# Performance work log

Measured on AMD Instinct MI355X. Metric: run time of the kernel, lower is better.

## Reference

```python
import jax, jax.numpy as jnp
import numpy as np

NOPE = 128          # qk_nope_head_dim
ROPE = 64           # qk_rope_head_dim
KV_LORA = 512       # kv_lora_rank
SCALE = (KV_LORA + ROPE) ** (-0.5)


def setup_inputs() -> dict:
    key = jax.random.key(0)
    k1, k2, k3, k4, k5 = jax.random.split(key, 5)
    T, H, K, S = 512, 128, 512, 8192
    q = jax.random.normal(k1, (T, H, NOPE + ROPE), dtype=jnp.float32)
    kv_cache = jax.random.normal(k2, (S, KV_LORA + ROPE), dtype=jnp.float32)
    topk_indices = jax.random.randint(k3, (T, K), 0, S, dtype=jnp.int32)
    k_b_proj_trans = jax.random.normal(k4, (H, KV_LORA, NOPE), dtype=jnp.float32) * 0.02
    v_b_proj = jax.random.normal(k5, (H, 128, KV_LORA), dtype=jnp.float32) * 0.02
    return {"q": q, "kv_cache": kv_cache, "topk_indices": topk_indices,
            "k_b_proj_trans": k_b_proj_trans, "v_b_proj": v_b_proj}


def reference(q, kv_cache, topk_indices, k_b_proj_trans, v_b_proj):
    # q: [T, H, 192]; kv_cache: [S, 576]; topk_indices: [T, K]
    q_nope, q_rope = q[..., :NOPE], q[..., NOPE:]
    # bmm_out(q_nope_t, k_b_proj_trans.transpose(1,2)): [T,H,128] x [H,512,128] -> [T,H,512]
    q_lat = jnp.einsum('thd,hkd->thk', q_nope, k_b_proj_trans)
    q_concat = jnp.concatenate([q_lat, q_rope], axis=-1)        # [T, H, 576]
    # sparse MLA: gather selected latent KV per token
    kv_sel = kv_cache[topk_indices]                              # [T, K, 576]
    scores = jnp.einsum('thc,tkc->thk', q_concat, kv_sel) * SCALE
    p = jax.nn.softmax(scores, axis=-1)                          # [T, H, K]
    attn_lat = jnp.einsum('thk,tkc->thc', p, kv_sel[..., :KV_LORA])  # [T, H, 512]
    # bmm_out(attn_lat_t, v_b_proj.transpose(1,2)): [T,H,512] x [H,512,128] -> [T,H,128]
    out = jnp.einsum('thc,hvc->thv', attn_lat, v_b_proj)
    return out
```

## Files before the change

kernel.cpp:

```cpp
#include <hip/hip_runtime.h>
#include <stdint.h>


#define SCALE 0.041666666666666664f

typedef __bf16 bf16x8 __attribute__((ext_vector_type(8)));
typedef float floatx4 __attribute__((ext_vector_type(4)));
typedef unsigned int uint32x2 __attribute__((ext_vector_type(2)));
typedef unsigned int uint32x4 __attribute__((ext_vector_type(4)));

static __device__ __forceinline__ unsigned short f2bf(float f) {
  unsigned int u = __builtin_bit_cast(unsigned int, f);
  u += 0x7FFF + ((u >> 16) & 1);
  return (unsigned short)(u >> 16);
}
static __device__ __forceinline__ float bf2f(unsigned short h) {
  unsigned int u = ((unsigned int)h) << 16;
  return __builtin_bit_cast(float, u);
}
static __device__ __forceinline__ unsigned int pack2(float lo, float hi) {
  return (unsigned int)f2bf(lo) | ((unsigned int)f2bf(hi) << 16);
}
static __device__ __forceinline__ void ldsdma16(const void* g, void* l) {
  __builtin_amdgcn_global_load_lds(
      (const __attribute__((address_space(1))) void*)g,
      (__attribute__((address_space(3))) void*)l, 16, 0, 0);
}
static __device__ __forceinline__ void issue_fence() {
  asm volatile("" ::: "memory");
  __builtin_amdgcn_sched_barrier(0);
}
static __device__ __forceinline__ unsigned int lds_addr(const void* p) {
  return (unsigned int)(unsigned long long)(
      (__attribute__((address_space(3))) const void*)p);
}
#define TR64(dst, addr, OFF) \
  asm volatile("ds_read_b64_tr_b16 %0, %1 offset:" OFF : "=v"(dst) : "v"(addr))

static __device__ __forceinline__ void stage8_f32(const float* __restrict__ src,
                                                  unsigned short* dst) {
  const float4* s4 = reinterpret_cast<const float4*>(src);
  float4 v0 = s4[0], v1 = s4[1];
  uint4 o;
  o.x = pack2(v0.x, v0.y); o.y = pack2(v0.z, v0.w);
  o.z = pack2(v1.x, v1.y); o.w = pack2(v1.z, v1.w);
  *reinterpret_cast<uint4*>(dst) = o;
}

static __device__ __forceinline__ void mfma_4x4(const unsigned short* As,
                                                const unsigned short* Bs,
                                                int wm, int wn, int l15, int quad,
                                                floatx4 acc[4][4]) {
  bf16x8 af[4], bfr[4];
#pragma unroll
  for (int i = 0; i < 4; ++i)
    af[i] = *reinterpret_cast<const bf16x8*>(&As[(wm + i * 16 + l15) * 32 + quad * 8]);
#pragma unroll
  for (int j = 0; j < 4; ++j)
    bfr[j] = *reinterpret_cast<const bf16x8*>(&Bs[(wn + j * 16 + l15) * 32 + quad * 8]);
#pragma unroll
  for (int i = 0; i < 4; ++i)
#pragma unroll
    for (int j = 0; j < 4; ++j)
      acc[i][j] = __builtin_amdgcn_mfma_f32_16x16x32_bf16(af[i], bfr[j], acc[i][j], 0, 0, 0);
}

__global__ void prep(const float* __restrict__ kv, unsigned short* __restrict__ kvb,
                     const float* __restrict__ q, unsigned short* __restrict__ qc2) {
  int b = blockIdx.x;
  if (b < 4608) {
    int i = b * 256 + threadIdx.x;
    float4 v = reinterpret_cast<const float4*>(kv)[i];
    ushort4 o;
    o.x = f2bf(v.x); o.y = f2bf(v.y); o.z = f2bf(v.z); o.w = f2bf(v.w);
    reinterpret_cast<ushort4*>(kvb)[i] = o;
  } else {
    int i = (b - 4608) * 256 + threadIdx.x;
    int r = i & 63;
    int th = i >> 6;
    int t = th >> 7, h = th & 127;
    qc2[(((size_t)t * 18 + 16 + (r >> 5)) * 128 + h) * 32 + (r & 31)] =
        f2bf(q[(size_t)th * 192 + 128 + r] * SCALE);
  }
}

__global__ __launch_bounds__(256) void qlat_gemm(const float* __restrict__ q,
                                                 const float* __restrict__ kb,
                                                 unsigned short* __restrict__ qc2) {
  const int h = blockIdx.x;
  const int tm = (blockIdx.y & 3) * 128;
  const int tn = (blockIdx.y >> 2) * 128;
  __shared__ __align__(16) unsigned short As[128 * 32];
  __shared__ __align__(16) unsigned short Bs[128 * 32];
  const int tid = threadIdx.x;
  const int lane = tid & 63, wave = tid >> 6;
  const int wm = (wave & 1) * 64, wn = (wave >> 1) * 64;
  const int l15 = lane & 15, quad = lane >> 4;
  const int r0 = tid >> 2, cg = tid & 3;
  const float* a0 = q + ((size_t)(tm + r0) * 128 + h) * 192 + cg * 8;
  const float* a1 = q + ((size_t)(tm + r0 + 64) * 128 + h) * 192 + cg * 8;
  const float* b0 = kb + ((size_t)h * 512 + tn + r0) * 128 + cg * 8;
  const float* b1 = b0 + (size_t)64 * 128;
  floatx4 acc[4][4] = {};
  for (int ks = 0; ks < 4; ++ks) {
    stage8_f32(a0 + ks * 32, &As[tid * 8]);
    stage8_f32(a1 + ks * 32, &As[2048 + tid * 8]);
    stage8_f32(b0 + ks * 32, &Bs[tid * 8]);
    stage8_f32(b1 + ks * 32, &Bs[2048 + tid * 8]);
    __syncthreads();
    mfma_4x4(As, Bs, wm, wn, l15, quad, acc);
    __syncthreads();
  }
#pragma unroll
  for (int i = 0; i < 4; ++i) {
    const int row = wm + i * 16 + quad * 4;
#pragma unroll
    for (int j = 0; j < 4; ++j) {
      const int c = tn + wn + j * 16 + l15;
      const int ks2 = c >> 5, kk = c & 31;
#pragma unroll
      for (int r = 0; r < 4; ++r) {
        const int t = tm + row + r;
        qc2[(((size_t)t * 18 + ks2) * 128 + h) * 32 + kk] = f2bf(acc[i][j][r] * SCALE);
      }
    }
  }
}

__global__ __launch_bounds__(512) void scores_fused(const unsigned short* __restrict__ qc2,
                                                    const unsigned short* __restrict__ kvb,
                                                    const int* __restrict__ topk,
                                                    unsigned short* __restrict__ P2) {
  const int t = blockIdx.x;
  __shared__ __align__(16) unsigned short Bs[3][512 * 32];
  __shared__ __align__(16) float redmx[128][4];
  __shared__ __align__(16) float redsm[128][4];
  const int tid = threadIdx.x;
  const int lane = tid & 63, wave = tid >> 6;
  const int wm2 = (wave >> 2) * 64;
  const int wkn = (wave & 3) * 128;
  const int l15 = lane & 15, quad = lane >> 4;
  const int keyD = tid >> 2;
  const int cD = (tid & 3) * 8;
  const int* tkrow = topk + t * 512;
  const int gi0 = tkrow[0 * 128 + keyD];
  const int gi1 = tkrow[1 * 128 + keyD];
  const int gi2 = tkrow[2 * 128 + keyD];
  const int gi3 = tkrow[3 * 128 + keyD];
  const unsigned short* g0 = kvb + (size_t)gi0 * 576 + cD;
  const unsigned short* g1 = kvb + (size_t)gi1 * 576 + cD;
  const unsigned short* g2 = kvb + (size_t)gi2 * 576 + cD;
  const unsigned short* g3 = kvb + (size_t)gi3 * 576 + cD;
  const unsigned short* aab =
      qc2 + ((size_t)t * 2304 + wm2 + l15) * 32 + quad * 8;
  floatx4 acc[4][8] = {};
  ldsdma16(g0, &Bs[0][0 * 4096 + tid * 8]);
  ldsdma16(g1, &Bs[0][1 * 4096 + tid * 8]);
  ldsdma16(g2, &Bs[0][2 * 4096 + tid * 8]);
  ldsdma16(g3, &Bs[0][3 * 4096 + tid * 8]);
  issue_fence();
  ldsdma16(g0 + 32, &Bs[1][0 * 4096 + tid * 8]);
  ldsdma16(g1 + 32, &Bs[1][1 * 4096 + tid * 8]);
  ldsdma16(g2 + 32, &Bs[1][2 * 4096 + tid * 8]);
  ldsdma16(g3 + 32, &Bs[1][3 * 4096 + tid * 8]);
  issue_fence();
  bf16x8 af[4], an[4];
#pragma unroll
  for (int i = 0; i < 4; ++i)
    af[i] = *reinterpret_cast<const bf16x8*>(aab + i * 512);
  int bi = 0, bn = 2;
  for (int ks = 0; ks < 18; ++ks) {
    asm volatile("s_waitcnt vmcnt(8)" ::: "memory");
    __builtin_amdgcn_s_barrier();
    if (ks < 16) {
      ldsdma16(g0 + (ks + 2) * 32, &Bs[bn][0 * 4096 + tid * 8]);
      ldsdma16(g1 + (ks + 2) * 32, &Bs[bn][1 * 4096 + tid * 8]);
      ldsdma16(g2 + (ks + 2) * 32, &Bs[bn][2 * 4096 + tid * 8]);
      ldsdma16(g3 + (ks + 2) * 32, &Bs[bn][3 * 4096 + tid * 8]);
      issue_fence();
    }
    if (ks < 17) {
#pragma unroll
      for (int i = 0; i < 4; ++i)
        an[i] = *reinterpret_cast<const bf16x8*>(
            aab + (size_t)(ks + 1) * 4096 + i * 512);
    }
    bf16x8 bfr[8];
#pragma unroll
    for (int j = 0; j < 8; ++j)
      bfr[j] = *reinterpret_cast<const bf16x8*>(
          &Bs[bi][(wkn + j * 16 + l15) * 32 + quad * 8]);
#pragma unroll
    for (int i = 0; i < 4; ++i)
#pragma unroll
      for (int j = 0; j < 8; ++j)
        acc[i][j] =
            __builtin_amdgcn_mfma_f32_16x16x32_bf16(af[i], bfr[j], acc[i][j], 0, 0, 0);
#pragma unroll
    for (int i = 0; i < 4; ++i) af[i] = an[i];
    bi = bi == 2 ? 0 : bi + 1;
    bn = bn == 2 ? 0 : bn + 1;
  }
  float fm[4][4], inv[4][4];
#pragma unroll
  for (int i = 0; i < 4; ++i)
#pragma unroll
    for (int r = 0; r < 4; ++r) {
      float m = acc[i][0][r];
#pragma unroll
      for (int j = 1; j < 8; ++j) m = fmaxf(m, acc[i][j][r]);
#pragma unroll
      for (int off = 1; off <= 8; off <<= 1) m = fmaxf(m, __shfl_xor(m, off, 64));
      if (l15 == 0) redmx[wm2 + i * 16 + quad * 4 + r][wave & 3] = m;
    }
  __syncthreads();
#pragma unroll
  for (int i = 0; i < 4; ++i)
#pragma unroll
    for (int r = 0; r < 4; ++r) {
      const float4 q4 =
          *reinterpret_cast<const float4*>(redmx[wm2 + i * 16 + quad * 4 + r]);
      fm[i][r] = fmaxf(fmaxf(q4.x, q4.y), fmaxf(q4.z, q4.w));
    }
#pragma unroll
  for (int i = 0; i < 4; ++i)
#pragma unroll
    for (int r = 0; r < 4; ++r) {
      float s = 0.f;
#pragma unroll
      for (int j = 0; j < 8; ++j) {
        const float e = __expf(acc[i][j][r] - fm[i][r]);
        acc[i][j][r] = e;
        s += e;
      }
#pragma unroll
      for (int off = 1; off <= 8; off <<= 1) s += __shfl_xor(s, off, 64);
      if (l15 == 0) redsm[wm2 + i * 16 + quad * 4 + r][wave & 3] = s;
    }
  __syncthreads();
#pragma unroll
  for (int i = 0; i < 4; ++i)
#pragma unroll
    for (int r = 0; r < 4; ++r) {
      const float4 q4 =
          *reinterpret_cast<const float4*>(redsm[wm2 + i * 16 + quad * 4 + r]);
      inv[i][r] = 1.0f / (q4.x + q4.y + q4.z + q4.w);
    }
#pragma unroll
  for (int i = 0; i < 4; ++i)
#pragma unroll
    for (int j = 0; j < 8; ++j) {
      const int ks2 = (wave & 3) * 4 + (j >> 1);
      const int co = (j & 1) * 16 + l15;
#pragma unroll
      for (int r = 0; r < 4; ++r) {
        const int head = wm2 + i * 16 + quad * 4 + r;
        P2[(((size_t)t * 16 + ks2) * 128 + head) * 32 + co] =
            f2bf(acc[i][j][r] * inv[i][r]);
      }
    }
}

__global__ __launch_bounds__(512) void attn_gemm(const unsigned short* __restrict__ P2,
                                                 const unsigned short* __restrict__ kvb,
                                                 const int* __restrict__ topk,
                                                 unsigned short* __restrict__ alat2) {
  const int t = blockIdx.x;
  __shared__ __align__(16) unsigned short St[3][32 * 512];
  const int tid = threadIdx.x;
  const int lane = tid & 63, wave = tid >> 6;
  const int wm = (wave >> 2) * 64;
  const int wc = wave & 3;
  const int l15 = lane & 15, quad = lane >> 4;
  const int keyBase = (tid >> 8) * 4 + ((tid >> 1) & 3);
  const int cA = ((tid >> 3) & 31) * 16 + (tid & 1) * 8;
  const int* tkrow = topk + t * 512;
  const unsigned short* a_base =
      P2 + ((size_t)t * 16 * 128 + wm + l15) * 32 + quad * 8;
  const unsigned int tra0 = lds_addr(&St[0][0]) + quad * 8192 + wc * 1024 + l15 * 8;
  floatx4 acc[4][8] = {};
  bf16x8 a_cur[4], a_nxt[4];
  int ip0, ip1, ip2, ip3;
  {
#pragma unroll
    for (int d = 0; d < 4; ++d) {
      const int k0 = tkrow[d * 8 + keyBase];
      ldsdma16(kvb + (size_t)k0 * 576 + cA, &St[0][d * 4096 + tid * 8]);
    }
#pragma unroll
    for (int i = 0; i < 4; ++i)
      a_cur[i] = *reinterpret_cast<const bf16x8*>(a_base + (size_t)i * 16 * 32);
    ip0 = tkrow[64 + 0 * 8 + keyBase];
    ip1 = tkrow[64 + 1 * 8 + keyBase];
    ip2 = tkrow[64 + 2 * 8 + keyBase];
    ip3 = tkrow[64 + 3 * 8 + keyBase];
    issue_fence();
#pragma unroll
    for (int d = 0; d < 4; ++d) {
      const int k1 = tkrow[32 + d * 8 + keyBase];
      ldsdma16(kvb + (size_t)k1 * 576 + cA, &St[1][d * 4096 + tid * 8]);
    }
  }
  int sti = 0, stp = 2;
  for (int ks = 0; ks < 16; ++ks) {
    asm volatile("s_waitcnt vmcnt(4)" ::: "memory");
    __builtin_amdgcn_s_barrier();
    const unsigned int tra = tra0 + sti * 32768;
    uint32x2 rl0, rl1, rl2, rl3, rl4, rl5, rl6, rl7;
    uint32x2 rh0, rh1, rh2, rh3, rh4, rh5, rh6, rh7;
    TR64(rl0, tra, "0");    TR64(rh0, tra, "4096");
    TR64(rl1, tra, "128");  TR64(rh1, tra, "4224");
    TR64(rl2, tra, "256");  TR64(rh2, tra, "4352");
    TR64(rl3, tra, "384");  TR64(rh3, tra, "4480");
    TR64(rl4, tra, "512");  TR64(rh4, tra, "4608");
    TR64(rl5, tra, "640");  TR64(rh5, tra, "4736");
    TR64(rl6, tra, "768");  TR64(rh6, tra, "4864");
    TR64(rl7, tra, "896");  TR64(rh7, tra, "4992");
    if (ks < 15) {
#pragma unroll
      for (int i = 0; i < 4; ++i)
        a_nxt[i] = *reinterpret_cast<const bf16x8*>(
            a_base + ((size_t)(ks + 1) * 128 + i * 16) * 32);
    }
    if (ks < 14) {
      const int d0 = ip0, d1 = ip1, d2 = ip2, d3 = ip3;
      if (ks < 13) {
        ip0 = tkrow[(ks + 3) * 32 + 0 * 8 + keyBase];
        ip1 = tkrow[(ks + 3) * 32 + 1 * 8 + keyBase];
        ip2 = tkrow[(ks + 3) * 32 + 2 * 8 + keyBase];
        ip3 = tkrow[(ks + 3) * 32 + 3 * 8 + keyBase];
      }
      issue_fence();
      ldsdma16(kvb + (size_t)d0 * 576 + cA, &St[stp][0 * 4096 + tid * 8]);
      ldsdma16(kvb + (size_t)d1 * 576 + cA, &St[stp][1 * 4096 + tid * 8]);
      ldsdma16(kvb + (size_t)d2 * 576 + cA, &St[stp][2 * 4096 + tid * 8]);
      ldsdma16(kvb + (size_t)d3 * 576 + cA, &St[stp][3 * 4096 + tid * 8]);
    }
    asm volatile("s_waitcnt lgkmcnt(0)");
    __builtin_amdgcn_sched_barrier(0);
    bf16x8 bfr[8];
    {
      uint32x4 w;
      w.x = rl0.x; w.y = rl0.y; w.z = rh0.x; w.w = rh0.y; bfr[0] = __builtin_bit_cast(bf16x8, w);
      w.x = rl1.x; w.y = rl1.y; w.z = rh1.x; w.w = rh1.y; bfr[1] = __builtin_bit_cast(bf16x8, w);
      w.x = rl2.x; w.y = rl2.y; w.z = rh2.x; w.w = rh2.y; bfr[2] = __builtin_bit_cast(bf16x8, w);
      w.x = rl3.x; w.y = rl3.y; w.z = rh3.x; w.w = rh3.y; bfr[3] = __builtin_bit_cast(bf16x8, w);
      w.x = rl4.x; w.y = rl4.y; w.z = rh4.x; w.w = rh4.y; bfr[4] = __builtin_bit_cast(bf16x8, w);
      w.x = rl5.x; w.y = rl5.y; w.z = rh5.x; w.w = rh5.y; bfr[5] = __builtin_bit_cast(bf16x8, w);
      w.x = rl6.x; w.y = rl6.y; w.z = rh6.x; w.w = rh6.y; bfr[6] = __builtin_bit_cast(bf16x8, w);
      w.x = rl7.x; w.y = rl7.y; w.z = rh7.x; w.w = rh7.y; bfr[7] = __builtin_bit_cast(bf16x8, w);
    }
#pragma unroll
    for (int i = 0; i < 4; ++i)
#pragma unroll
      for (int j = 0; j < 8; ++j)
        acc[i][j] =
            __builtin_amdgcn_mfma_f32_16x16x32_bf16(a_cur[i], bfr[j], acc[i][j], 0, 0, 0);
#pragma unroll
    for (int i = 0; i < 4; ++i) a_cur[i] = a_nxt[i];
    sti = sti == 2 ? 0 : sti + 1;
    stp = stp == 2 ? 0 : stp + 1;
  }
#pragma unroll
  for (int i = 0; i < 4; ++i) {
    const int row = wm + i * 16 + quad * 4;
#pragma unroll
    for (int j = 0; j < 8; ++j) {
      const int c = wc * 128 + j * 16 + l15;
      const int ks2 = c >> 5, kk = c & 31;
#pragma unroll
      for (int r = 0; r < 4; ++r)
        alat2[(((size_t)(row + r) * 16 + ks2) * 512 + t) * 32 + kk] =
            f2bf(acc[i][j][r]);
    }
  }
}

__global__ __launch_bounds__(256) void out_gemm(const unsigned short* __restrict__ alat2,
                                                const float* __restrict__ vb,
                                                float* __restrict__ out) {
  const int h = blockIdx.x;
  const int tm = blockIdx.y * 128;
  __shared__ __align__(16) unsigned short Bs[128 * 32];
  const int tid = threadIdx.x;
  const int lane = tid & 63, wave = tid >> 6;
  const int wm = (wave & 1) * 64, wn = (wave >> 1) * 64;
  const int l15 = lane & 15, quad = lane >> 4;
  const int r0 = tid >> 2, cg = tid & 3;
  const unsigned short* aab =
      alat2 + ((size_t)h * 8192 + tm + wm + l15) * 32 + quad * 8;
  const float* b0 = vb + ((size_t)h * 128 + r0) * 512 + cg * 8;
  const float* b1 = b0 + (size_t)64 * 512;
  floatx4 acc[4][4] = {};
  for (int ks = 0; ks < 16; ++ks) {
    stage8_f32(b0 + ks * 32, &Bs[tid * 8]);
    stage8_f32(b1 + ks * 32, &Bs[2048 + tid * 8]);
    __syncthreads();
    bf16x8 af[4], bfr[4];
#pragma unroll
    for (int i = 0; i < 4; ++i)
      af[i] = *reinterpret_cast<const bf16x8*>(
          aab + (size_t)ks * 16384 + i * 512);
#pragma unroll
    for (int j = 0; j < 4; ++j)
      bfr[j] = *reinterpret_cast<const bf16x8*>(
          &Bs[(wn + j * 16 + l15) * 32 + quad * 8]);
#pragma unroll
    for (int i = 0; i < 4; ++i)
#pragma unroll
      for (int j = 0; j < 4; ++j)
        acc[i][j] =
            __builtin_amdgcn_mfma_f32_16x16x32_bf16(af[i], bfr[j], acc[i][j], 0, 0, 0);
    __syncthreads();
  }
#pragma unroll
  for (int i = 0; i < 4; ++i) {
    const int row = wm + i * 16 + quad * 4;
#pragma unroll
    for (int j = 0; j < 4; ++j) {
      const int col = wn + j * 16 + l15;
#pragma unroll
      for (int r = 0; r < 4; ++r) {
        const int t = tm + row + r;
        out[((size_t)t * 128 + h) * 128 + col] = acc[i][j][r];
      }
    }
  }
}

extern "C" void kernel_launch(void* const* d_in, const int* in_sizes, int n_in,
                              void* d_out, int out_size, void* d_ws, size_t ws_size,
                              hipStream_t stream) {
  const float* q = (const float*)d_in[0];
  const float* kv = (const float*)d_in[1];
  const int* topk = (const int*)d_in[2];
  const float* kb = (const float*)d_in[3];
  const float* vb = (const float*)d_in[4];
  float* out = (float*)d_out;

  char* ws = (char*)d_ws;
  unsigned short* kvb = (unsigned short*)ws;
  unsigned short* qc2 = (unsigned short*)(ws + 9437184);
  unsigned short* P2 = (unsigned short*)(ws + 9437184 + 75497472);
  unsigned short* alat2 = qc2;

  prep<<<dim3(20992), dim3(256), 0, stream>>>(kv, kvb, q, qc2);
  qlat_gemm<<<dim3(128, 16), dim3(256), 0, stream>>>(q, kb, qc2);
  scores_fused<<<dim3(512), dim3(512), 0, stream>>>(qc2, kvb, topk, P2);
  attn_gemm<<<dim3(512), dim3(512), 0, stream>>>(P2, kvb, topk, alat2);
  out_gemm<<<dim3(128, 4), dim3(256), 0, stream>>>(alat2, vb, out);
}
```

Measured before the change: 361.9 us.

## Use 1024-thread blocks with smaller per-wave tiles and double buffering in attention kernels

```diff
diff --git a/kernel.cpp b/kernel.cpp
--- a/kernel.cpp
+++ b/kernel.cpp
@@ -127,83 +127,59 @@
   }
 }
 
-__global__ __launch_bounds__(512) void scores_fused(const unsigned short* __restrict__ qc2,
-                                                    const unsigned short* __restrict__ kvb,
-                                                    const int* __restrict__ topk,
-                                                    unsigned short* __restrict__ P2) {
+__global__ __launch_bounds__(1024) void scores_fused(const unsigned short* __restrict__ qc2,
+                                                     const unsigned short* __restrict__ kvb,
+                                                     const int* __restrict__ topk,
+                                                     unsigned short* __restrict__ P2) {
   const int t = blockIdx.x;
-  __shared__ __align__(16) unsigned short Bs[3][512 * 32];
+  __shared__ __align__(16) unsigned short Bs[2][512 * 32];
   __shared__ __align__(16) float redmx[128][4];
   __shared__ __align__(16) float redsm[128][4];
   const int tid = threadIdx.x;
   const int lane = tid & 63, wave = tid >> 6;
-  const int wm2 = (wave >> 2) * 64;
-  const int wkn = (wave & 3) * 128;
+  const int wm2 = (wave >> 2) * 32;
+  const int wkq = wave & 3;
   const int l15 = lane & 15, quad = lane >> 4;
   const int keyD = tid >> 2;
   const int cD = (tid & 3) * 8;
   const int* tkrow = topk + t * 512;
-  const int gi0 = tkrow[0 * 128 + keyD];
-  const int gi1 = tkrow[1 * 128 + keyD];
-  const int gi2 = tkrow[2 * 128 + keyD];
-  const int gi3 = tkrow[3 * 128 + keyD];
+  const int gi0 = tkrow[keyD];
+  const int gi1 = tkrow[256 + keyD];
   const unsigned short* g0 = kvb + (size_t)gi0 * 576 + cD;
   const unsigned short* g1 = kvb + (size_t)gi1 * 576 + cD;
-  const unsigned short* g2 = kvb + (size_t)gi2 * 576 + cD;
-  const unsigned short* g3 = kvb + (size_t)gi3 * 576 + cD;
   const unsigned short* aab =
       qc2 + ((size_t)t * 2304 + wm2 + l15) * 32 + quad * 8;
-  floatx4 acc[4][8] = {};
-  ldsdma16(g0, &Bs[0][0 * 4096 + tid * 8]);
-  ldsdma16(g1, &Bs[0][1 * 4096 + tid * 8]);
-  ldsdma16(g2, &Bs[0][2 * 4096 + tid * 8]);
-  ldsdma16(g3, &Bs[0][3 * 4096 + tid * 8]);
+  floatx4 acc[2][8] = {};
+  ldsdma16(g0, &Bs[0][tid * 8]);
+  ldsdma16(g1, &Bs[0][8192 + tid * 8]);
   issue_fence();
-  ldsdma16(g0 + 32, &Bs[1][0 * 4096 + tid * 8]);
-  ldsdma16(g1 + 32, &Bs[1][1 * 4096 + tid * 8]);
-  ldsdma16(g2 + 32, &Bs[1][2 * 4096 + tid * 8]);
-  ldsdma16(g3 + 32, &Bs[1][3 * 4096 + tid * 8]);
-  issue_fence();
-  bf16x8 af[4], an[4];
-#pragma unroll
-  for (int i = 0; i < 4; ++i)
-    af[i] = *reinterpret_cast<const bf16x8*>(aab + i * 512);
-  int bi = 0, bn = 2;
+  bf16x8 af[2], an[2];
+  af[0] = *reinterpret_cast<const bf16x8*>(aab);
+  af[1] = *reinterpret_cast<const bf16x8*>(aab + 512);
   for (int ks = 0; ks < 18; ++ks) {
-    asm volatile("s_waitcnt vmcnt(8)" ::: "memory");
+    asm volatile("s_waitcnt vmcnt(2)" ::: "memory");
     __builtin_amdgcn_s_barrier();
-    if (ks < 16) {
-      ldsdma16(g0 + (ks + 2) * 32, &Bs[bn][0 * 4096 + tid * 8]);
-      ldsdma16(g1 + (ks + 2) * 32, &Bs[bn][1 * 4096 + tid * 8]);
-      ldsdma16(g2 + (ks + 2) * 32, &Bs[bn][2 * 4096 + tid * 8]);
-      ldsdma16(g3 + (ks + 2) * 32, &Bs[bn][3 * 4096 + tid * 8]);
+    if (ks < 17) {
+      ldsdma16(g0 + (ks + 1) * 32, &Bs[(ks + 1) & 1][tid * 8]);
+      ldsdma16(g1 + (ks + 1) * 32, &Bs[(ks + 1) & 1][8192 + tid * 8]);
       issue_fence();
-    }
-    if (ks < 17) {
-#pragma unroll
-      for (int i = 0; i < 4; ++i)
-        an[i] = *reinterpret_cast<const bf16x8*>(
-            aab + (size_t)(ks + 1) * 4096 + i * 512);
-    }
-    bf16x8 bfr[8];
-#pragma unroll
-    for (int j = 0; j < 8; ++j)
-      bfr[j] = *reinterpret_cast<const bf16x8*>(
-          &Bs[bi][(wkn + j * 16 + l15) * 32 + quad * 8]);
-#pragma unroll
-    for (int i = 0; i < 4; ++i)
-#pragma unroll
-      for (int j = 0; j < 8; ++j)
-        acc[i][j] =
-            __builtin_amdgcn_mfma_f32_16x16x32_bf16(af[i], bfr[j], acc[i][j], 0, 0, 0);
-#pragma unroll
-    for (int i = 0; i < 4; ++i) af[i] = an[i];
-    bi = bi == 2 ? 0 : bi + 1;
-    bn = bn == 2 ? 0 : bn + 1;
-  }
-  float fm[4][4], inv[4][4];
-#pragma unroll
-  for (int i = 0; i < 4; ++i)
+      an[0] = *reinterpret_cast<const bf16x8*>(aab + (size_t)(ks + 1) * 4096);
+      an[1] = *reinterpret_cast<const bf16x8*>(aab + (size_t)(ks + 1) * 4096 + 512);
+    }
+    const unsigned short* bb = &Bs[ks & 1][0];
+#pragma unroll
+    for (int j = 0; j < 8; ++j) {
+      const bf16x8 bfr = *reinterpret_cast<const bf16x8*>(
+          &bb[(wkq * 128 + j * 16 + l15) * 32 + quad * 8]);
+      acc[0][j] = __builtin_amdgcn_mfma_f32_16x16x32_bf16(af[0], bfr, acc[0][j], 0, 0, 0);
+      acc[1][j] = __builtin_amdgcn_mfma_f32_16x16x32_bf16(af[1], bfr, acc[1][j], 0, 0, 0);
+    }
+    af[0] = an[0];
+    af[1] = an[1];
+  }
+  float fm[2][4], inv[2][4];
+#pragma unroll
+  for (int i = 0; i < 2; ++i)
 #pragma unroll
     for (int r = 0; r < 4; ++r) {
       float m = acc[i][0][r];
@@ -211,11 +187,11 @@
       for (int j = 1; j < 8; ++j) m = fmaxf(m, acc[i][j][r]);
 #pragma unroll
       for (int off = 1; off <= 8; off <<= 1) m = fmaxf(m, __shfl_xor(m, off, 64));
-      if (l15 == 0) redmx[wm2 + i * 16 + quad * 4 + r][wave & 3] = m;
+      if (l15 == 0) redmx[wm2 + i * 16 + quad * 4 + r][wkq] = m;
     }
   __syncthreads();
 #pragma unroll
-  for (int i = 0; i < 4; ++i)
+  for (int i = 0; i < 2; ++i)
 #pragma unroll
     for (int r = 0; r < 4; ++r) {
       const float4 q4 =
@@ -223,7 +199,7 @@
       fm[i][r] = fmaxf(fmaxf(q4.x, q4.y), fmaxf(q4.z, q4.w));
     }
 #pragma unroll
-  for (int i = 0; i < 4; ++i)
+  for (int i = 0; i < 2; ++i)
 #pragma unroll
     for (int r = 0; r < 4; ++r) {
       float s = 0.f;
@@ -235,11 +211,11 @@
       }
 #pragma unroll
       for (int off = 1; off <= 8; off <<= 1) s += __shfl_xor(s, off, 64);
-      if (l15 == 0) redsm[wm2 + i * 16 + quad * 4 + r][wave & 3] = s;
+      if (l15 == 0) redsm[wm2 + i * 16 + quad * 4 + r][wkq] = s;
     }
   __syncthreads();
 #pragma unroll
-  for (int i = 0; i < 4; ++i)
+  for (int i = 0; i < 2; ++i)
 #pragma unroll
     for (int r = 0; r < 4; ++r) {
       const float4 q4 =
@@ -247,10 +223,10 @@
       inv[i][r] = 1.0f / (q4.x + q4.y + q4.z + q4.w);
     }
 #pragma unroll
-  for (int i = 0; i < 4; ++i)
+  for (int i = 0; i < 2; ++i)
 #pragma unroll
     for (int j = 0; j < 8; ++j) {
-      const int ks2 = (wave & 3) * 4 + (j >> 1);
+      const int ks2 = wkq * 4 + (j >> 1);
       const int co = (j & 1) * 16 + l15;
 #pragma unroll
       for (int r = 0; r < 4; ++r) {
@@ -261,108 +237,105 @@
     }
 }
 
-__global__ __launch_bounds__(512) void attn_gemm(const unsigned short* __restrict__ P2,
-                                                 const unsigned short* __restrict__ kvb,
-                                                 const int* __restrict__ topk,
-                                                 unsigned short* __restrict__ alat2) {
+__global__ __launch_bounds__(1024) void attn_gemm(const unsigned short* __restrict__ P2,
+                                                  const unsigned short* __restrict__ kvb,
+                                                  const int* __restrict__ topk,
+                                                  unsigned short* __restrict__ alat2) {
   const int t = blockIdx.x;
-  __shared__ __align__(16) unsigned short St[3][32 * 512];
+  __shared__ __align__(16) unsigned short St[2][32 * 512];
   const int tid = threadIdx.x;
   const int lane = tid & 63, wave = tid >> 6;
-  const int wm = (wave >> 2) * 64;
+  const int wm = (wave >> 2) * 32;
   const int wc = wave & 3;
   const int l15 = lane & 15, quad = lane >> 4;
-  const int keyBase = (tid >> 8) * 4 + ((tid >> 1) & 3);
+  const int kb2 = (tid >> 8) * 4 + ((tid >> 1) & 3);
   const int cA = ((tid >> 3) & 31) * 16 + (tid & 1) * 8;
   const int* tkrow = topk + t * 512;
   const unsigned short* a_base =
-      P2 + ((size_t)t * 16 * 128 + wm + l15) * 32 + quad * 8;
+      P2 + ((size_t)t * 2048 + wm + l15) * 32 + quad * 8;
   const unsigned int tra0 = lds_addr(&St[0][0]) + quad * 8192 + wc * 1024 + l15 * 8;
-  floatx4 acc[4][8] = {};
-  bf16x8 a_cur[4], a_nxt[4];
-  int ip0, ip1, ip2, ip3;
+  floatx4 acc[2][8] = {};
+  bf16x8 a_cur[2], a_nxt[2];
+  int ip0, ip1;
   {
-#pragma unroll
-    for (int d = 0; d < 4; ++d) {
-      const int k0 = tkrow[d * 8 + keyBase];
-      ldsdma16(kvb + (size_t)k0 * 576 + cA, &St[0][d * 4096 + tid * 8]);
-    }
-#pragma unroll
-    for (int i = 0; i < 4; ++i)
-      a_cur[i] = *reinterpret_cast<const bf16x8*>(a_base + (size_t)i * 16 * 32);
-    ip0 = tkrow[64 + 0 * 8 + keyBase];
-    ip1 = tkrow[64 + 1 * 8 + keyBase];
-    ip2 = tkrow[64 + 2 * 8 + keyBase];
-    ip3 = tkrow[64 + 3 * 8 + keyBase];
+    const int k00 = tkrow[kb2];
+    const int k01 = tkrow[16 + kb2];
+    ldsdma16(kvb + (size_t)k00 * 576 + cA, &St[0][tid * 8]);
+    ldsdma16(kvb + (size_t)k01 * 576 + cA, &St[0][8192 + tid * 8]);
     issue_fence();
-#pragma unroll
-    for (int d = 0; d < 4; ++d) {
-      const int k1 = tkrow[32 + d * 8 + keyBase];
-      ldsdma16(kvb + (size_t)k1 * 576 + cA, &St[1][d * 4096 + tid * 8]);
-    }
-  }
-  int sti = 0, stp = 2;
+    a_cur[0] = *reinterpret_cast<const bf16x8*>(a_base);
+    a_cur[1] = *reinterpret_cast<const bf16x8*>(a_base + 512);
+    ip0 = tkrow[32 + kb2];
+    ip1 = tkrow[48 + kb2];
+    issue_fence();
+  }
   for (int ks = 0; ks < 16; ++ks) {
-    asm volatile("s_waitcnt vmcnt(4)" ::: "memory");
+    if (ks < 15) asm volatile("s_waitcnt vmcnt(4)" ::: "memory");
+    else         asm volatile("s_waitcnt vmcnt(2)" ::: "memory");
     __builtin_amdgcn_s_barrier();
-    const unsigned int tra = tra0 + sti * 32768;
-    uint32x2 rl0, rl1, rl2, rl3, rl4, rl5, rl6, rl7;
-    uint32x2 rh0, rh1, rh2, rh3, rh4, rh5, rh6, rh7;
-    TR64(rl0, tra, "0");    TR64(rh0, tra, "4096");
-    TR64(rl1, tra, "128");  TR64(rh1, tra, "4224");
-    TR64(rl2, tra, "256");  TR64(rh2, tra, "4352");
-    TR64(rl3, tra, "384");  TR64(rh3, tra, "4480");
-    TR64(rl4, tra, "512");  TR64(rh4, tra, "4608");
-    TR64(rl5, tra, "640");  TR64(rh5, tra, "4736");
-    TR64(rl6, tra, "768");  TR64(rh6, tra, "4864");
-    TR64(rl7, tra, "896");  TR64(rh7, tra, "4992");
+    const unsigned int tra = tra0 + (ks & 1) * 32768;
     if (ks < 15) {
-#pragma unroll
-      for (int i = 0; i < 4; ++i)
-        a_nxt[i] = *reinterpret_cast<const bf16x8*>(
-            a_base + ((size_t)(ks + 1) * 128 + i * 16) * 32);
-    }
-    if (ks < 14) {
-      const int d0 = ip0, d1 = ip1, d2 = ip2, d3 = ip3;
-      if (ks < 13) {
-        ip0 = tkrow[(ks + 3) * 32 + 0 * 8 + keyBase];
-        ip1 = tkrow[(ks + 3) * 32 + 1 * 8 + keyBase];
-        ip2 = tkrow[(ks + 3) * 32 + 2 * 8 + keyBase];
-        ip3 = tkrow[(ks + 3) * 32 + 3 * 8 + keyBase];
+      ldsdma16(kvb + (size_t)ip0 * 576 + cA, &St[(ks + 1) & 1][tid * 8]);
+      ldsdma16(kvb + (size_t)ip1 * 576 + cA, &St[(ks + 1) & 1][8192 + tid * 8]);
+      issue_fence();
+      a_nxt[0] = *reinterpret_cast<const bf16x8*>(a_base + (size_t)(ks + 1) * 4096);
+      a_nxt[1] = *reinterpret_cast<const bf16x8*>(a_base + (size_t)(ks + 1) * 4096 + 512);
+      if (ks < 14) {
+        ip0 = tkrow[(ks + 2) * 32 + kb2];
+        ip1 = tkrow[(ks + 2) * 32 + 16 + kb2];
       }
-      issue_fence();
-      ldsdma16(kvb + (size_t)d0 * 576 + cA, &St[stp][0 * 4096 + tid * 8]);
-      ldsdma16(kvb + (size_t)d1 * 576 + cA, &St[stp][1 * 4096 + tid * 8]);
-      ldsdma16(kvb + (size_t)d2 * 576 + cA, &St[stp][2 * 4096 + tid * 8]);
-      ldsdma16(kvb + (size_t)d3 * 576 + cA, &St[stp][3 * 4096 + tid * 8]);
-    }
-    asm volatile("s_waitcnt lgkmcnt(0)");
-    __builtin_amdgcn_sched_barrier(0);
-    bf16x8 bfr[8];
+    }
     {
+      uint32x2 rl0, rl1, rl2, rl3, rh0, rh1, rh2, rh3;
+      TR64(rl0, tra, "0");    TR64(rh0, tra, "4096");
+      TR64(rl1, tra, "128");  TR64(rh1, tra, "4224");
+      TR64(rl2, tra, "256");  TR64(rh2, tra, "4352");
+      TR64(rl3, tra, "384");  TR64(rh3, tra, "4480");
+      asm volatile("s_waitcnt lgkmcnt(0)");
+      __builtin_amdgcn_sched_barrier(0);
       uint32x4 w;
-      w.x = rl0.x; w.y = rl0.y; w.z = rh0.x; w.w = rh0.y; bfr[0] = __builtin_bit_cast(bf16x8, w);
-      w.x = rl1.x; w.y = rl1.y; w.z = rh1.x; w.w = rh1.y; bfr[1] = __builtin_bit_cast(bf16x8, w);
-      w.x = rl2.x; w.y = rl2.y; w.z = rh2.x; w.w = rh2.y; bfr[2] = __builtin_bit_cast(bf16x8, w);
-      w.x = rl3.x; w.y = rl3.y; w.z = rh3.x; w.w = rh3.y; bfr[3] = __builtin_bit_cast(bf16x8, w);
-      w.x = rl4.x; w.y = rl4.y; w.z = rh4.x; w.w = rh4.y; bfr[4] = __builtin_bit_cast(bf16x8, w);
-      w.x = rl5.x; w.y = rl5.y; w.z = rh5.x; w.w = rh5.y; bfr[5] = __builtin_bit_cast(bf16x8, w);
-      w.x = rl6.x; w.y = rl6.y; w.z = rh6.x; w.w = rh6.y; bfr[6] = __builtin_bit_cast(bf16x8, w);
-      w.x = rl7.x; w.y = rl7.y; w.z = rh7.x; w.w = rh7.y; bfr[7] = __builtin_bit_cast(bf16x8, w);
-    }
-#pragma unroll
-    for (int i = 0; i < 4; ++i)
-#pragma unroll
-      for (int j = 0; j < 8; ++j)
-        acc[i][j] =
-            __builtin_amdgcn_mfma_f32_16x16x32_bf16(a_cur[i], bfr[j], acc[i][j], 0, 0, 0);
-#pragma unroll
-    for (int i = 0; i < 4; ++i) a_cur[i] = a_nxt[i];
-    sti = sti == 2 ? 0 : sti + 1;
-    stp = stp == 2 ? 0 : stp + 1;
-  }
-#pragma unroll
-  for (int i = 0; i < 4; ++i) {
+      bf16x8 bfr;
+      w.x = rl0.x; w.y = rl0.y; w.z = rh0.x; w.w = rh0.y; bfr = __builtin_bit_cast(bf16x8, w);
+      acc[0][0] = __builtin_amdgcn_mfma_f32_16x16x32_bf16(a_cur[0], bfr, acc[0][0], 0, 0, 0);
+      acc[1][0] = __builtin_amdgcn_mfma_f32_16x16x32_bf16(a_cur[1], bfr, acc[1][0], 0, 0, 0);
+      w.x = rl1.x; w.y = rl1.y; w.z = rh1.x; w.w = rh1.y; bfr = __builtin_bit_cast(bf16x8, w);
+      acc[0][1] = __builtin_amdgcn_mfma_f32_16x16x32_bf16(a_cur[0], bfr, acc[0][1], 0, 0, 0);
+      acc[1][1] = __builtin_amdgcn_mfma_f32_16x16x32_bf16(a_cur[1], bfr, acc[1][1], 0, 0, 0);
+      w.x = rl2.x; w.y = rl2.y; w.z = rh2.x; w.w = rh2.y; bfr = __builtin_bit_cast(bf16x8, w);
+      acc[0][2] = __builtin_amdgcn_mfma_f32_16x16x32_bf16(a_cur[0], bfr, acc[0][2], 0, 0, 0);
+      acc[1][2] = __builtin_amdgcn_mfma_f32_16x16x32_bf16(a_cur[1], bfr, acc[1][2], 0, 0, 0);
+      w.x = rl3.x; w.y = rl3.y; w.z = rh3.x; w.w = rh3.y; bfr = __builtin_bit_cast(bf16x8, w);
+      acc[0][3] = __builtin_amdgcn_mfma_f32_16x16x32_bf16(a_cur[0], bfr, acc[0][3], 0, 0, 0);
+      acc[1][3] = __builtin_amdgcn_mfma_f32_16x16x32_bf16(a_cur[1], bfr, acc[1][3], 0, 0, 0);
+    }
+    {
+      uint32x2 rl4, rl5, rl6, rl7, rh4, rh5, rh6, rh7;
+      TR64(rl4, tra, "512");  TR64(rh4, tra, "4608");
+      TR64(rl5, tra, "640");  TR64(rh5, tra, "4736");
+      TR64(rl6, tra, "768");  TR64(rh6, tra, "4864");
+      TR64(rl7, tra, "896");  TR64(rh7, tra, "4992");
+      asm volatile("s_waitcnt lgkmcnt(0)");
+      __builtin_amdgcn_sched_barrier(0);
+      uint32x4 w;
+      bf16x8 bfr;
+      w.x = rl4.x; w.y = rl4.y; w.z = rh4.x; w.w = rh4.y; bfr = __builtin_bit_cast(bf16x8, w);
+      acc[0][4] = __builtin_amdgcn_mfma_f32_16x16x32_bf16(a_cur[0], bfr, acc[0][4], 0, 0, 0);
+      acc[1][4] = __builtin_amdgcn_mfma_f32_16x16x32_bf16(a_cur[1], bfr, acc[1][4], 0, 0, 0);
+      w.x = rl5.x; w.y = rl5.y; w.z = rh5.x; w.w = rh5.y; bfr = __builtin_bit_cast(bf16x8, w);
+      acc[0][5] = __builtin_amdgcn_mfma_f32_16x16x32_bf16(a_cur[0], bfr, acc[0][5], 0, 0, 0);
+      acc[1][5] = __builtin_amdgcn_mfma_f32_16x16x32_bf16(a_cur[1], bfr, acc[1][5], 0, 0, 0);
+      w.x = rl6.x; w.y = rl6.y; w.z = rh6.x; w.w = rh6.y; bfr = __builtin_bit_cast(bf16x8, w);
+      acc[0][6] = __builtin_amdgcn_mfma_f32_16x16x32_bf16(a_cur[0], bfr, acc[0][6], 0, 0, 0);
+      acc[1][6] = __builtin_amdgcn_mfma_f32_16x16x32_bf16(a_cur[1], bfr, acc[1][6], 0, 0, 0);
+      w.x = rl7.x; w.y = rl7.y; w.z = rh7.x; w.w = rh7.y; bfr = __builtin_bit_cast(bf16x8, w);
+      acc[0][7] = __builtin_amdgcn_mfma_f32_16x16x32_bf16(a_cur[0], bfr, acc[0][7], 0, 0, 0);
+      acc[1][7] = __builtin_amdgcn_mfma_f32_16x16x32_bf16(a_cur[1], bfr, acc[1][7], 0, 0, 0);
+    }
+    a_cur[0] = a_nxt[0];
+    a_cur[1] = a_nxt[1];
+  }
+#pragma unroll
+  for (int i = 0; i < 2; ++i) {
     const int row = wm + i * 16 + quad * 4;
 #pragma unroll
     for (int j = 0; j < 8; ++j) {
@@ -446,7 +419,7 @@
 
   prep<<<dim3(20992), dim3(256), 0, stream>>>(kv, kvb, q, qc2);
   qlat_gemm<<<dim3(128, 16), dim3(256), 0, stream>>>(q, kb, qc2);
-  scores_fused<<<dim3(512), dim3(512), 0, stream>>>(qc2, kvb, topk, P2);
-  attn_gemm<<<dim3(512), dim3(512), 0, stream>>>(P2, kvb, topk, alat2);
+  scores_fused<<<dim3(512), dim3(1024), 0, stream>>>(qc2, kvb, topk, P2);
+  attn_gemm<<<dim3(512), dim3(1024), 0, stream>>>(P2, kvb, topk, alat2);
   out_gemm<<<dim3(128, 4), dim3(256), 0, stream>>>(alat2, vb, out);
 }
```

Result: faster. 352.9 us (-2.5%).

## Switch scores and attn kernels from triple to double LDS buffering

Applied to the files above, without the earlier changes.

```diff
diff --git a/kernel.cpp b/kernel.cpp
--- a/kernel.cpp
+++ b/kernel.cpp
@@ -132,13 +132,13 @@
                                                     const int* __restrict__ topk,
                                                     unsigned short* __restrict__ P2) {
   const int t = blockIdx.x;
-  __shared__ __align__(16) unsigned short Bs[3][512 * 32];
+  __shared__ __align__(16) unsigned short Bs[2][512 * 32];
   __shared__ __align__(16) float redmx[128][4];
   __shared__ __align__(16) float redsm[128][4];
   const int tid = threadIdx.x;
   const int lane = tid & 63, wave = tid >> 6;
   const int wm2 = (wave >> 2) * 64;
-  const int wkn = (wave & 3) * 128;
+  const int wkq = wave & 3;
   const int l15 = lane & 15, quad = lane >> 4;
   const int keyD = tid >> 2;
   const int cD = (tid & 3) * 8;
@@ -159,47 +159,36 @@
   ldsdma16(g2, &Bs[0][2 * 4096 + tid * 8]);
   ldsdma16(g3, &Bs[0][3 * 4096 + tid * 8]);
   issue_fence();
-  ldsdma16(g0 + 32, &Bs[1][0 * 4096 + tid * 8]);
-  ldsdma16(g1 + 32, &Bs[1][1 * 4096 + tid * 8]);
-  ldsdma16(g2 + 32, &Bs[1][2 * 4096 + tid * 8]);
-  ldsdma16(g3 + 32, &Bs[1][3 * 4096 + tid * 8]);
-  issue_fence();
   bf16x8 af[4], an[4];
 #pragma unroll
   for (int i = 0; i < 4; ++i)
     af[i] = *reinterpret_cast<const bf16x8*>(aab + i * 512);
-  int bi = 0, bn = 2;
   for (int ks = 0; ks < 18; ++ks) {
-    asm volatile("s_waitcnt vmcnt(8)" ::: "memory");
+    asm volatile("s_waitcnt vmcnt(4)" ::: "memory");
     __builtin_amdgcn_s_barrier();
-    if (ks < 16) {
-      ldsdma16(g0 + (ks + 2) * 32, &Bs[bn][0 * 4096 + tid * 8]);
-      ldsdma16(g1 + (ks + 2) * 32, &Bs[bn][1 * 4096 + tid * 8]);
-      ldsdma16(g2 + (ks + 2) * 32, &Bs[bn][2 * 4096 + tid * 8]);
-      ldsdma16(g3 + (ks + 2) * 32, &Bs[bn][3 * 4096 + tid * 8]);
+    if (ks < 17) {
+      const int nb = (ks + 1) & 1;
+      ldsdma16(g0 + (ks + 1) * 32, &Bs[nb][0 * 4096 + tid * 8]);
+      ldsdma16(g1 + (ks + 1) * 32, &Bs[nb][1 * 4096 + tid * 8]);
+      ldsdma16(g2 + (ks + 1) * 32, &Bs[nb][2 * 4096 + tid * 8]);
+      ldsdma16(g3 + (ks + 1) * 32, &Bs[nb][3 * 4096 + tid * 8]);
       issue_fence();
-    }
-    if (ks < 17) {
 #pragma unroll
       for (int i = 0; i < 4; ++i)
         an[i] = *reinterpret_cast<const bf16x8*>(
             aab + (size_t)(ks + 1) * 4096 + i * 512);
     }
-    bf16x8 bfr[8];
-#pragma unroll
-    for (int j = 0; j < 8; ++j)
-      bfr[j] = *reinterpret_cast<const bf16x8*>(
-          &Bs[bi][(wkn + j * 16 + l15) * 32 + quad * 8]);
-#pragma unroll
-    for (int i = 0; i < 4; ++i)
-#pragma unroll
-      for (int j = 0; j < 8; ++j)
-        acc[i][j] =
-            __builtin_amdgcn_mfma_f32_16x16x32_bf16(af[i], bfr[j], acc[i][j], 0, 0, 0);
+    const unsigned short* bb = &Bs[ks & 1][0];
+#pragma unroll
+    for (int j = 0; j < 8; ++j) {
+      const bf16x8 bfr = *reinterpret_cast<const bf16x8*>(
+          &bb[(wkq * 128 + j * 16 + l15) * 32 + quad * 8]);
+#pragma unroll
+      for (int i = 0; i < 4; ++i)
+        acc[i][j] = __builtin_amdgcn_mfma_f32_16x16x32_bf16(af[i], bfr, acc[i][j], 0, 0, 0);
+    }
 #pragma unroll
     for (int i = 0; i < 4; ++i) af[i] = an[i];
-    bi = bi == 2 ? 0 : bi + 1;
-    bn = bn == 2 ? 0 : bn + 1;
   }
   float fm[4][4], inv[4][4];
 #pragma unroll
@@ -211,7 +200,7 @@
       for (int j = 1; j < 8; ++j) m = fmaxf(m, acc[i][j][r]);
 #pragma unroll
       for (int off = 1; off <= 8; off <<= 1) m = fmaxf(m, __shfl_xor(m, off, 64));
-      if (l15 == 0) redmx[wm2 + i * 16 + quad * 4 + r][wave & 3] = m;
+      if (l15 == 0) redmx[wm2 + i * 16 + quad * 4 + r][wkq] = m;
     }
   __syncthreads();
 #pragma unroll
@@ -235,7 +224,7 @@
       }
 #pragma unroll
       for (int off = 1; off <= 8; off <<= 1) s += __shfl_xor(s, off, 64);
-      if (l15 == 0) redsm[wm2 + i * 16 + quad * 4 + r][wave & 3] = s;
+      if (l15 == 0) redsm[wm2 + i * 16 + quad * 4 + r][wkq] = s;
     }
   __syncthreads();
 #pragma unroll
@@ -250,7 +239,7 @@
   for (int i = 0; i < 4; ++i)
 #pragma unroll
     for (int j = 0; j < 8; ++j) {
-      const int ks2 = (wave & 3) * 4 + (j >> 1);
+      const int ks2 = wkq * 4 + (j >> 1);
       const int co = (j & 1) * 16 + l15;
 #pragma unroll
       for (int r = 0; r < 4; ++r) {
@@ -266,7 +255,7 @@
                                                  const int* __restrict__ topk,
                                                  unsigned short* __restrict__ alat2) {
   const int t = blockIdx.x;
-  __shared__ __align__(16) unsigned short St[3][32 * 512];
+  __shared__ __align__(16) unsigned short St[2][32 * 512];
   const int tid = threadIdx.x;
   const int lane = tid & 63, wave = tid >> 6;
   const int wm = (wave >> 2) * 64;
@@ -276,7 +265,7 @@
   const int cA = ((tid >> 3) & 31) * 16 + (tid & 1) * 8;
   const int* tkrow = topk + t * 512;
   const unsigned short* a_base =
-      P2 + ((size_t)t * 16 * 128 + wm + l15) * 32 + quad * 8;
+      P2 + ((size_t)t * 2048 + wm + l15) * 32 + quad * 8;
   const unsigned int tra0 = lds_addr(&St[0][0]) + quad * 8192 + wc * 1024 + l15 * 8;
   floatx4 acc[4][8] = {};
   bf16x8 a_cur[4], a_nxt[4];
@@ -287,25 +276,38 @@
       const int k0 = tkrow[d * 8 + keyBase];
       ldsdma16(kvb + (size_t)k0 * 576 + cA, &St[0][d * 4096 + tid * 8]);
     }
+    issue_fence();
 #pragma unroll
     for (int i = 0; i < 4; ++i)
       a_cur[i] = *reinterpret_cast<const bf16x8*>(a_base + (size_t)i * 16 * 32);
-    ip0 = tkrow[64 + 0 * 8 + keyBase];
-    ip1 = tkrow[64 + 1 * 8 + keyBase];
-    ip2 = tkrow[64 + 2 * 8 + keyBase];
-    ip3 = tkrow[64 + 3 * 8 + keyBase];
-    issue_fence();
-#pragma unroll
-    for (int d = 0; d < 4; ++d) {
-      const int k1 = tkrow[32 + d * 8 + keyBase];
-      ldsdma16(kvb + (size_t)k1 * 576 + cA, &St[1][d * 4096 + tid * 8]);
-    }
-  }
-  int sti = 0, stp = 2;
+    ip0 = tkrow[32 + 0 * 8 + keyBase];
+    ip1 = tkrow[32 + 1 * 8 + keyBase];
+    ip2 = tkrow[32 + 2 * 8 + keyBase];
+    ip3 = tkrow[32 + 3 * 8 + keyBase];
+  }
   for (int ks = 0; ks < 16; ++ks) {
-    asm volatile("s_waitcnt vmcnt(4)" ::: "memory");
+    if (ks < 15) asm volatile("s_waitcnt vmcnt(8)" ::: "memory");
+    else         asm volatile("s_waitcnt vmcnt(4)" ::: "memory");
     __builtin_amdgcn_s_barrier();
-    const unsigned int tra = tra0 + sti * 32768;
+    const unsigned int tra = tra0 + (ks & 1) * 32768;
+    if (ks < 15) {
+      const int nb = (ks + 1) & 1;
+      ldsdma16(kvb + (size_t)ip0 * 576 + cA, &St[nb][0 * 4096 + tid * 8]);
+      ldsdma16(kvb + (size_t)ip1 * 576 + cA, &St[nb][1 * 4096 + tid * 8]);
+      ldsdma16(kvb + (size_t)ip2 * 576 + cA, &St[nb][2 * 4096 + tid * 8]);
+      ldsdma16(kvb + (size_t)ip3 * 576 + cA, &St[nb][3 * 4096 + tid * 8]);
+      issue_fence();
+#pragma unroll
+      for (int i = 0; i < 4; ++i)
+        a_nxt[i] = *reinterpret_cast<const bf16x8*>(
+            a_base + ((size_t)(ks + 1) * 128 + i * 16) * 32);
+      if (ks < 14) {
+        ip0 = tkrow[(ks + 2) * 32 + 0 * 8 + keyBase];
+        ip1 = tkrow[(ks + 2) * 32 + 1 * 8 + keyBase];
+        ip2 = tkrow[(ks + 2) * 32 + 2 * 8 + keyBase];
+        ip3 = tkrow[(ks + 2) * 32 + 3 * 8 + keyBase];
+      }
+    }
     uint32x2 rl0, rl1, rl2, rl3, rl4, rl5, rl6, rl7;
     uint32x2 rh0, rh1, rh2, rh3, rh4, rh5, rh6, rh7;
     TR64(rl0, tra, "0");    TR64(rh0, tra, "4096");
@@ -316,26 +318,6 @@
     TR64(rl5, tra, "640");  TR64(rh5, tra, "4736");
     TR64(rl6, tra, "768");  TR64(rh6, tra, "4864");
     TR64(rl7, tra, "896");  TR64(rh7, tra, "4992");
-    if (ks < 15) {
-#pragma unroll
-      for (int i = 0; i < 4; ++i)
-        a_nxt[i] = *reinterpret_cast<const bf16x8*>(
-            a_base + ((size_t)(ks + 1) * 128 + i * 16) * 32);
-    }
-    if (ks < 14) {
-      const int d0 = ip0, d1 = ip1, d2 = ip2, d3 = ip3;
-      if (ks < 13) {
-        ip0 = tkrow[(ks + 3) * 32 + 0 * 8 + keyBase];
-        ip1 = tkrow[(ks + 3) * 32 + 1 * 8 + keyBase];
-        ip2 = tkrow[(ks + 3) * 32 + 2 * 8 + keyBase];
-        ip3 = tkrow[(ks + 3) * 32 + 3 * 8 + keyBase];
-      }
-      issue_fence();
-      ldsdma16(kvb + (size_t)d0 * 576 + cA, &St[stp][0 * 4096 + tid * 8]);
-      ldsdma16(kvb + (size_t)d1 * 576 + cA, &St[stp][1 * 4096 + tid * 8]);
-      ldsdma16(kvb + (size_t)d2 * 576 + cA, &St[stp][2 * 4096 + tid * 8]);
-      ldsdma16(kvb + (size_t)d3 * 576 + cA, &St[stp][3 * 4096 + tid * 8]);
-    }
     asm volatile("s_waitcnt lgkmcnt(0)");
     __builtin_amdgcn_sched_barrier(0);
     bf16x8 bfr[8];
@@ -358,8 +340,6 @@
             __builtin_amdgcn_mfma_f32_16x16x32_bf16(a_cur[i], bfr[j], acc[i][j], 0, 0, 0);
 #pragma unroll
     for (int i = 0; i < 4; ++i) a_cur[i] = a_nxt[i];
-    sti = sti == 2 ? 0 : sti + 1;
-    stp = stp == 2 ? 0 : stp + 1;
   }
 #pragma unroll
   for (int i = 0; i < 4; ++i) {
```

After: 365.2 us. Within noise of the previous version (+0.9%).
